# Kernel optimization log

Measured on AMD Instinct MI355X. Metric: run time of the kernel, lower is better.

Reference implementation:

```python
import jax, jax.numpy as jnp
import numpy as np

B, T, IN, H, OUT = 2048, 4096, 1, 8, 1


def setup_inputs() -> dict:
    key = jax.random.key(0)
    ks = jax.random.split(key, 11)
    s_in = 1.0 / np.sqrt(H)  # torch nn.LSTM/Linear init scale (uniform +-1/sqrt(H))
    u = lambda k, shape, s: jax.random.uniform(k, shape, jnp.float32, -s, s)
    return {
        "input_seq": jax.random.normal(ks[0], (B, T, IN), jnp.float32),
        # layer 0 (input_size=IN)
        "W_ih0": u(ks[1], (4 * H, IN), s_in),
        "W_hh0": u(ks[2], (4 * H, H), s_in),
        "b_ih0": u(ks[3], (4 * H,), s_in),
        "b_hh0": u(ks[4], (4 * H,), s_in),
        # layer 1 (input_size=H)
        "W_ih1": u(ks[5], (4 * H, H), s_in),
        "W_hh1": u(ks[6], (4 * H, H), s_in),
        "b_ih1": u(ks[7], (4 * H,), s_in),
        "b_hh1": u(ks[8], (4 * H,), s_in),
        # output projection
        "W_lin": u(ks[9], (OUT, H), s_in),
        "b_lin": u(ks[10], (OUT,), s_in),
    }


def _lstm_layer(x_tbi, W_ih, W_hh, b_ih, b_hh):
    """x_tbi: [T, B, in] -> hidden sequence [T, B, H]. PyTorch gate order i,f,g,o."""
    h_dim = W_hh.shape[1]
    # precompute input contribution for all timesteps (hoisted out of the scan)
    xg = jnp.einsum('tbi,gi->tbg', x_tbi, W_ih) + (b_ih + b_hh)  # [T, B, 4H]
    bsz = x_tbi.shape[1]
    h0 = jnp.zeros((bsz, h_dim), x_tbi.dtype)
    c0 = jnp.zeros((bsz, h_dim), x_tbi.dtype)

    def step(carry, xg_t):
        h, c = carry
        gates = xg_t + h @ W_hh.T  # [B, 4H]
        i, f, g, o = jnp.split(gates, 4, axis=-1)
        i = jax.nn.sigmoid(i)
        f = jax.nn.sigmoid(f)
        g = jnp.tanh(g)
        o = jax.nn.sigmoid(o)
        c = f * c + i * g
        h = o * jnp.tanh(c)
        return (h, c), h

    _, hs = jax.lax.scan(step, (h0, c0), xg)
    return hs  # [T, B, H]


def reference(input_seq, W_ih0, W_hh0, b_ih0, b_hh0,
              W_ih1, W_hh1, b_ih1, b_hh1, W_lin, b_lin):
    x = jnp.transpose(input_seq, (1, 0, 2))  # [T, B, IN] (batch_first -> time-major)
    h1 = _lstm_layer(x, W_ih0, W_hh0, b_ih0, b_hh0)   # [T, B, H]
    h2 = _lstm_layer(h1, W_ih1, W_hh1, b_ih1, b_hh1)  # [T, B, H]
    out = jnp.transpose(h2, (1, 0, 2))                # [B, T, H]
    pred = out @ W_lin.T + b_lin                      # [B, T, OUT]
    return pred
```

## Files before the change

kernel.cpp:

```cpp
#include <hip/hip_runtime.h>


constexpr int Bsz = 2048;
constexpr int Tsz = 4096;

typedef int v2i __attribute__((ext_vector_type(2)));

template <int CTRL>
__device__ __forceinline__ float dpp(float v) {
    return __int_as_float(
        __builtin_amdgcn_mov_dpp(__float_as_int(v), CTRL, 0xF, 0xF, true));
}

__device__ __forceinline__ float xchg16(float v, bool hi16) {
    const int vi = __float_as_int(v);
    v2i p = __builtin_amdgcn_permlane16_swap(vi, vi, false, false);
    return __int_as_float(hi16 ? p.x : p.y);
}

__device__ __forceinline__ float swz16(float v) {
    return __int_as_float(
        __builtin_amdgcn_ds_swizzle(__float_as_int(v), (16 << 10) | 0x1f));
}

__device__ __forceinline__ float bperm(int addr, float v) {
    return __int_as_float(__builtin_amdgcn_ds_bpermute(addr, __float_as_int(v)));
}

__global__ void __launch_bounds__(256, 2) lstm2_rr(
    const float* __restrict__ x,
    const float* __restrict__ Wih0,
    const float* __restrict__ Whh0,
    const float* __restrict__ bih0,
    const float* __restrict__ bhh0,
    const float* __restrict__ Wih1,
    const float* __restrict__ Whh1,
    const float* __restrict__ bih1,
    const float* __restrict__ bhh1,
    const float* __restrict__ Wlin,
    const float* __restrict__ blin,
    float* __restrict__ out)
{
    const int tid  = threadIdx.x;
    const int lane = tid & 63;
    const int g    = lane & 3;
    const int j    = (lane >> 2) & 7;
    const int L    = (lane >> 5) & 1;
    const int seq  = blockIdx.x * 4 + (tid >> 6);

    const int jm = j ^ 4;
    const int r  = g * 8 + j;
    const int rm = g * 8 + jm;

    const bool hi16 = (lane & 16) != 0;

    const float NL2E  = -1.4426950408889634f;
    const float N2L2E = -2.8853900817779268f;
    const bool  isG   = (g == 2);
    const float ws    = isG ? N2L2E : NL2E;
    const float sA    = isG ? 2.0f * N2L2E : 1.0f;
    const float oA    = isG ? -N2L2E : 0.0f;

    const float* __restrict__ Whh = L ? Whh1 : Whh0;
    const float* __restrict__ bih = L ? bih1 : bih0;
    const float* __restrict__ bhh = L ? bhh1 : bhh0;

    int u[4];
    u[0] = j;
    u[1] = (j & 4) | ((j + 3) & 3);
    u[2] = (j & 4) | ((j + 2) & 3);
    u[3] = (j & 4) | ((j + 1) & 3);

    float wn1[4], wm1[4], wn2[4], wm2[4];
#pragma unroll
    for (int i = 0; i < 4; ++i) {
        const int k = u[i];
        wn1[i] = Whh[r * 8 + k] * ws;
        wm1[i] = Whh[rm * 8 + k] * ws;
        wn2[i] = L ? Wlin[k] : Wih1[r * 8 + k] * ws;
        wm2[i] = L ? Wlin[k] : Wih1[rm * 8 + k] * ws;
    }
    const float bias = (bih[r] + bhh[r]) * ws;
    const float wx   = L ? 0.0f : Wih0[r] * ws;
    const float b2   = L ? blin[0] : 0.0f;
    const float mL   = L ? 1.0f : 0.0f;
    const float keep = 1.0f - mL;
    const int  xaddr = (lane ^ 32) * 4;

    const float* __restrict__ xp = x + (size_t)seq * Tsz;
    float* __restrict__ op       = out + (size_t)seq * Tsz;
    const bool storeLane = (lane == 32);

    float hn0 = 0.0f, hn1 = 0.0f, hn2 = 0.0f, hn3 = 0.0f;
    float cs = 0.0f;
    float recvP = 0.0f;
    float an2_hold = 0.0f;
    float s2p = 0.0f;

    auto body = [&](float xt, bool fill, float* storePtr) {
        const float d2 = an2_hold + s2p;
        if (storePtr && storeLane) *storePtr = d2;
        const float rB = recvP;
        recvP = bperm(xaddr, d2);
        const float t0 = fmaf(mL, rB, fmaf(wx, xt, bias));

        float am2 = wm2[0] * hn0;
        am2 = fmaf(wm2[1], hn1, am2);
        am2 = fmaf(wm2[2], hn2, am2);
        am2 = fmaf(wm2[3], hn3, am2);
        s2p = swz16(am2);

        float am1 = wm1[0] * hn0;
        am1 = fmaf(wm1[1], hn1, am1);
        am1 = fmaf(wm1[2], hn2, am1);
        am1 = fmaf(wm1[3], hn3, am1);
        const float s1 = xchg16(am1, hi16);

        float an1 = fmaf(wn1[0], hn0, t0);
        an1 = fmaf(wn1[1], hn1, an1);
        an1 = fmaf(wn1[2], hn2, an1);
        an1 = fmaf(wn1[3], hn3, an1);
        float an2 = fmaf(wn2[0], hn0, b2);
        an2 = fmaf(wn2[1], hn1, an2);
        an2 = fmaf(wn2[2], hn2, an2);
        an2 = fmaf(wn2[3], hn3, an2);
        an2_hold = an2;

        const float z = an1 + s1;

        float a = fmaf(sA,
                       __builtin_amdgcn_rcpf(1.0f + __builtin_amdgcn_exp2f(z)),
                       oA);
        const float gi = dpp<0x00>(a);
        const float gf = dpp<0x55>(a);
        const float gG = dpp<0xAA>(a);
        const float go = dpp<0xFF>(a);
        const float go2 = go + go;
        cs = fmaf(gf, cs, gi * gG);
        const float e  = __builtin_amdgcn_exp2f(cs);
        const float rr = __builtin_amdgcn_rcpf(1.0f + e);
        float h = fmaf(go2, rr, -go);

        if (fill) { h *= keep; cs *= keep; }

        hn0 = h;
        hn1 = dpp<0x124>(h);
        hn2 = dpp<0x128>(h);
        hn3 = dpp<0x12C>(h);
    };

    body(xp[0], true, nullptr);
    body(xp[1], true, nullptr);
    body(xp[2], true, nullptr);
    body(xp[3], false, nullptr);
    body(xp[4], false, nullptr);

    float xc[4];
#pragma unroll
    for (int u2 = 0; u2 < 4; ++u2) xc[u2] = xp[5 + u2];
    for (int ck = 0; ck < Tsz / 4; ++ck) {
        const int base = 5 + 4 * ck;
        float xf[4];
#pragma unroll
        for (int u2 = 0; u2 < 4; ++u2) {
            int idx = base + 4 + u2;
            idx = (idx < Tsz) ? idx : (Tsz - 1);
            xf[u2] = xp[idx];
        }
#pragma unroll
        for (int u2 = 0; u2 < 4; ++u2)
            body(xc[u2], false, op + (4 * ck + u2));
#pragma unroll
        for (int u2 = 0; u2 < 4; ++u2) xc[u2] = xf[u2];
    }
}

extern "C" void kernel_launch(void* const* d_in, const int* in_sizes, int n_in,
                              void* d_out, int out_size, void* d_ws, size_t ws_size,
                              hipStream_t stream) {
    const float* x    = (const float*)d_in[0];
    const float* Wih0 = (const float*)d_in[1];
    const float* Whh0 = (const float*)d_in[2];
    const float* bih0 = (const float*)d_in[3];
    const float* bhh0 = (const float*)d_in[4];
    const float* Wih1 = (const float*)d_in[5];
    const float* Whh1 = (const float*)d_in[6];
    const float* bih1 = (const float*)d_in[7];
    const float* bhh1 = (const float*)d_in[8];
    const float* Wlin = (const float*)d_in[9];
    const float* blin = (const float*)d_in[10];
    float* out = (float*)d_out;

    dim3 grid(Bsz / 4);
    dim3 block(256);
    hipLaunchKernelGGL(lstm2_rr, grid, block, 0, stream,
                       x, Wih0, Whh0, bih0, bhh0,
                       Wih1, Whh1, bih1, bhh1, Wlin, blin, out);
}
```

Before: 842.1 us.

## Interleave two independent sequences per wavefront to hide recurrence latency

```diff
diff --git a/kernel.cpp b/kernel.cpp
--- a/kernel.cpp
+++ b/kernel.cpp
@@ -27,7 +27,15 @@
     return __int_as_float(__builtin_amdgcn_ds_bpermute(addr, __float_as_int(v)));
 }
 
-__global__ void __launch_bounds__(256, 2) lstm2_rr(
+struct St {
+    float hn0, hn1, hn2, hn3;
+    float cs;
+    float recvP;
+    float an2_hold;
+    float s2p;
+};
+
+__global__ void __launch_bounds__(256, 1) lstm2_i2(
     const float* __restrict__ x,
     const float* __restrict__ Wih0,
     const float* __restrict__ Whh0,
@@ -46,7 +54,7 @@
     const int g    = lane & 3;
     const int j    = (lane >> 2) & 7;
     const int L    = (lane >> 5) & 1;
-    const int seq  = blockIdx.x * 4 + (tid >> 6);
+    const int seq0 = (blockIdx.x * 4 + (tid >> 6)) * 2;
 
     const int jm = j ^ 4;
     const int r  = g * 8 + j;
@@ -87,44 +95,43 @@
     const float keep = 1.0f - mL;
     const int  xaddr = (lane ^ 32) * 4;
 
-    const float* __restrict__ xp = x + (size_t)seq * Tsz;
-    float* __restrict__ op       = out + (size_t)seq * Tsz;
+    const float* __restrict__ xpA = x + (size_t)seq0 * Tsz;
+    const float* __restrict__ xpB = xpA + Tsz;
+    float* __restrict__ opA       = out + (size_t)seq0 * Tsz;
+    float* __restrict__ opB       = opA + Tsz;
     const bool storeLane = (lane == 32);
 
-    float hn0 = 0.0f, hn1 = 0.0f, hn2 = 0.0f, hn3 = 0.0f;
-    float cs = 0.0f;
-    float recvP = 0.0f;
-    float an2_hold = 0.0f;
-    float s2p = 0.0f;
-
-    auto body = [&](float xt, bool fill, float* storePtr) {
-        const float d2 = an2_hold + s2p;
+    St A = {0, 0, 0, 0, 0, 0, 0, 0};
+    St B = {0, 0, 0, 0, 0, 0, 0, 0};
+
+    auto body = [&](St& S, float xt, bool fill, float* storePtr) {
+        const float d2 = S.an2_hold + S.s2p;
         if (storePtr && storeLane) *storePtr = d2;
-        const float rB = recvP;
-        recvP = bperm(xaddr, d2);
+        const float rB = S.recvP;
+        S.recvP = bperm(xaddr, d2);
         const float t0 = fmaf(mL, rB, fmaf(wx, xt, bias));
 
-        float am2 = wm2[0] * hn0;
-        am2 = fmaf(wm2[1], hn1, am2);
-        am2 = fmaf(wm2[2], hn2, am2);
-        am2 = fmaf(wm2[3], hn3, am2);
-        s2p = swz16(am2);
-
-        float am1 = wm1[0] * hn0;
-        am1 = fmaf(wm1[1], hn1, am1);
-        am1 = fmaf(wm1[2], hn2, am1);
-        am1 = fmaf(wm1[3], hn3, am1);
+        float am2 = wm2[0] * S.hn0;
+        am2 = fmaf(wm2[1], S.hn1, am2);
+        am2 = fmaf(wm2[2], S.hn2, am2);
+        am2 = fmaf(wm2[3], S.hn3, am2);
+        S.s2p = swz16(am2);
+
+        float am1 = wm1[0] * S.hn0;
+        am1 = fmaf(wm1[1], S.hn1, am1);
+        am1 = fmaf(wm1[2], S.hn2, am1);
+        am1 = fmaf(wm1[3], S.hn3, am1);
         const float s1 = xchg16(am1, hi16);
 
-        float an1 = fmaf(wn1[0], hn0, t0);
-        an1 = fmaf(wn1[1], hn1, an1);
-        an1 = fmaf(wn1[2], hn2, an1);
-        an1 = fmaf(wn1[3], hn3, an1);
-        float an2 = fmaf(wn2[0], hn0, b2);
-        an2 = fmaf(wn2[1], hn1, an2);
-        an2 = fmaf(wn2[2], hn2, an2);
-        an2 = fmaf(wn2[3], hn3, an2);
-        an2_hold = an2;
+        float an1 = fmaf(wn1[0], S.hn0, t0);
+        an1 = fmaf(wn1[1], S.hn1, an1);
+        an1 = fmaf(wn1[2], S.hn2, an1);
+        an1 = fmaf(wn1[3], S.hn3, an1);
+        float an2 = fmaf(wn2[0], S.hn0, b2);
+        an2 = fmaf(wn2[1], S.hn1, an2);
+        an2 = fmaf(wn2[2], S.hn2, an2);
+        an2 = fmaf(wn2[3], S.hn3, an2);
+        S.an2_hold = an2;
 
         const float z = an1 + s1;
 
@@ -136,42 +143,45 @@
         const float gG = dpp<0xAA>(a);
         const float go = dpp<0xFF>(a);
         const float go2 = go + go;
-        cs = fmaf(gf, cs, gi * gG);
-        const float e  = __builtin_amdgcn_exp2f(cs);
+        S.cs = fmaf(gf, S.cs, gi * gG);
+        const float e  = __builtin_amdgcn_exp2f(S.cs);
         const float rr = __builtin_amdgcn_rcpf(1.0f + e);
         float h = fmaf(go2, rr, -go);
 
-        if (fill) { h *= keep; cs *= keep; }
-
-        hn0 = h;
-        hn1 = dpp<0x124>(h);
-        hn2 = dpp<0x128>(h);
-        hn3 = dpp<0x12C>(h);
+        if (fill) { h *= keep; S.cs *= keep; }
+
+        S.hn0 = h;
+        S.hn1 = dpp<0x124>(h);
+        S.hn2 = dpp<0x128>(h);
+        S.hn3 = dpp<0x12C>(h);
     };
 
-    body(xp[0], true, nullptr);
-    body(xp[1], true, nullptr);
-    body(xp[2], true, nullptr);
-    body(xp[3], false, nullptr);
-    body(xp[4], false, nullptr);
-
-    float xc[4];
-#pragma unroll
-    for (int u2 = 0; u2 < 4; ++u2) xc[u2] = xp[5 + u2];
+    body(A, xpA[0], true,  nullptr);  body(B, xpB[0], true,  nullptr);
+    body(A, xpA[1], true,  nullptr);  body(B, xpB[1], true,  nullptr);
+    body(A, xpA[2], true,  nullptr);  body(B, xpB[2], true,  nullptr);
+    body(A, xpA[3], false, nullptr);  body(B, xpB[3], false, nullptr);
+    body(A, xpA[4], false, nullptr);  body(B, xpB[4], false, nullptr);
+
+    float xcA[4], xcB[4];
+#pragma unroll
+    for (int q = 0; q < 4; ++q) { xcA[q] = xpA[5 + q]; xcB[q] = xpB[5 + q]; }
     for (int ck = 0; ck < Tsz / 4; ++ck) {
         const int base = 5 + 4 * ck;
-        float xf[4];
-#pragma unroll
-        for (int u2 = 0; u2 < 4; ++u2) {
-            int idx = base + 4 + u2;
+        float xfA[4], xfB[4];
+#pragma unroll
+        for (int q = 0; q < 4; ++q) {
+            int idx = base + 4 + q;
             idx = (idx < Tsz) ? idx : (Tsz - 1);
-            xf[u2] = xp[idx];
+            xfA[q] = xpA[idx];
+            xfB[q] = xpB[idx];
         }
 #pragma unroll
-        for (int u2 = 0; u2 < 4; ++u2)
-            body(xc[u2], false, op + (4 * ck + u2));
-#pragma unroll
-        for (int u2 = 0; u2 < 4; ++u2) xc[u2] = xf[u2];
+        for (int q = 0; q < 4; ++q) {
+            body(A, xcA[q], false, opA + (4 * ck + q));
+            body(B, xcB[q], false, opB + (4 * ck + q));
+        }
+#pragma unroll
+        for (int q = 0; q < 4; ++q) { xcA[q] = xfA[q]; xcB[q] = xfB[q]; }
     }
 }
 
@@ -191,9 +201,9 @@
     const float* blin = (const float*)d_in[10];
     float* out = (float*)d_out;
 
-    dim3 grid(Bsz / 4);
+    dim3 grid(Bsz / 8);
     dim3 block(256);
-    hipLaunchKernelGGL(lstm2_rr, grid, block, 0, stream,
+    hipLaunchKernelGGL(lstm2_i2, grid, block, 0, stream,
                        x, Wih0, Whh0, bih0, bhh0,
                        Wih1, Whh1, bih1, bhh1, Wlin, blin, out);
 }
```

Result: slower. 1.134 ms (+34.6%).
